# Kernel optimization log

Hardware: AMD Instinct MI355X
Metric: run time of the kernel (lower is better)

## Reference

```python
import jax, jax.numpy as jnp
import numpy as np

D_MODEL = 3072
N_HEADS = 24
HEAD_DIM = D_MODEL // N_HEADS          # 128
Q_PROJ = D_MODEL // 2                  # 1536
KV_PROJ = 2 * D_MODEL // 3             # 2048
ROPE_DIM = HEAD_DIM // 2               # 64 (qk_rope_dim == qk_no_rope_dim)
MAX_LEN = 2048
ROPE_THETA = 10000.0
EPS = 1e-6
B, S = 2, 2048


def setup_inputs() -> dict:
    key = jax.random.key(0)
    ks = jax.random.split(key, 7)
    return {
        "x": jax.random.normal(ks[0], (B, S, D_MODEL), dtype=jnp.float32),
        "scale": jnp.ones((D_MODEL,), dtype=jnp.float32),
        "w_dq": 0.01 * jax.random.normal(ks[1], (D_MODEL, Q_PROJ), dtype=jnp.float32),
        "w_uq": 0.01 * jax.random.normal(ks[2], (Q_PROJ, D_MODEL), dtype=jnp.float32),
        "w_dkv": 0.01 * jax.random.normal(ks[3], (D_MODEL, KV_PROJ + ROPE_DIM), dtype=jnp.float32),
        "w_ukv": 0.01 * jax.random.normal(ks[4], (KV_PROJ, D_MODEL + N_HEADS * ROPE_DIM), dtype=jnp.float32),
        "w_o": 0.01 * jax.random.normal(ks[5], (D_MODEL, D_MODEL), dtype=jnp.float32),
    }


def _rope_cos_sin(seq_len):
    # freqs over full head_dim, sliced to rope_dim//2 then tiled x2 (as in torch repeat)
    freqs = 1.0 / (ROPE_THETA ** (jnp.arange(0, HEAD_DIM, 2, dtype=jnp.float32) / HEAD_DIM))
    angles = jnp.arange(seq_len, dtype=jnp.float32)[:, None] * freqs[None, :]  # [S, 64]
    ang = angles[:, : ROPE_DIM // 2]                                            # [S, 32]
    cos = jnp.tile(jnp.cos(ang), (1, 2))                                        # [S, 64]
    sin = jnp.tile(jnp.sin(ang), (1, 2))
    return cos[None, None], sin[None, None]  # [1,1,S,64]


def _rotate_half(t):
    a, b = jnp.split(t, 2, axis=-1)
    return jnp.concatenate([-b, a], axis=-1)


def reference(x, scale, w_dq, w_uq, w_dkv, w_ukv, w_o):
    b, s, _ = x.shape
    # RMSNorm pre-normalization
    xn = scale * (x * jax.lax.rsqrt(jnp.mean(x * x, axis=-1, keepdims=True) + EPS))
    # two-stage query projection
    q = (xn @ w_dq) @ w_uq                                   # [B,S,D]
    q = q.reshape(b, s, N_HEADS, HEAD_DIM).transpose(0, 2, 1, 3)  # [B,H,S,hd]
    q_no_rope, q_rope = jnp.split(q, [ROPE_DIM], axis=-1)
    cos, sin = _rope_cos_sin(s)
    q_rope = q_rope * cos + _rotate_half(q_rope) * sin
    # KV down projection (this is the kv cache)
    kv_down = xn @ w_dkv                                     # [B,S,KV_PROJ+rope]
    kv_no_rope, k_rope = jnp.split(kv_down, [KV_PROJ], axis=-1)
    # KV up projection
    kv_up = kv_no_rope @ w_ukv                               # [B,S,H*(hd+rope)]
    kv_up = kv_up.reshape(b, s, N_HEADS, HEAD_DIM + ROPE_DIM).transpose(0, 2, 1, 3)
    key, value = jnp.split(kv_up, [ROPE_DIM], axis=-1)       # key [B,H,S,64], value [B,H,S,128]
    # shared rope key (one head, broadcast to all heads)
    k_rope = k_rope[:, None, :, :]                           # [B,1,S,64]
    k_rope = k_rope * cos + _rotate_half(k_rope) * sin
    k_rope = jnp.broadcast_to(k_rope, (b, N_HEADS, s, ROPE_DIM))
    final_q = jnp.concatenate([q_no_rope, q_rope], axis=-1)  # [B,H,S,128]
    final_k = jnp.concatenate([key, k_rope], axis=-1)        # [B,H,S,128]
    # masked SDPA (causal, past_length=0)
    inv_scale = 1.0 / jnp.sqrt(jnp.asarray(HEAD_DIM, dtype=x.dtype))
    scores = jnp.einsum("bhsd,bhtd->bhst", final_q, final_k) * inv_scale
    causal = jnp.tril(jnp.ones((s, s), dtype=bool))
    scores = jnp.where(causal[None, None], scores, jnp.asarray(-1e30, dtype=scores.dtype))
    attn = jax.nn.softmax(scores, axis=-1)
    attn_out = jnp.einsum("bhst,bhtd->bhsd", attn, value)    # [B,H,S,128]
    attn_out = attn_out.transpose(0, 2, 1, 3).reshape(b, s, D_MODEL)
    output = attn_out @ w_o.T
    return output, kv_down
```

## Files before the change

### kernel.cpp

```cpp
#include <hip/hip_runtime.h>
#include <hip/hip_bf16.h>
#include <stdint.h>

using bf16_t = __bf16;
using bf16x8 = __attribute__((ext_vector_type(8))) __bf16;
using bf16x4 = __attribute__((ext_vector_type(4))) __bf16;
using f32x4  = __attribute__((ext_vector_type(4))) float;

#define D_MODEL 3072
#define N_HEADS 24
#define HEAD_DIM 128
#define Q_PROJ 1536
#define KV_PROJ 2048
#define ROPE_DIM 64
#define S_LEN 2048
#define NTOK 4096
#define KVDN 2112
#define KVUN 4608

__device__ __forceinline__ void async_ld16(const void* g, void* l) {
    __builtin_amdgcn_global_load_lds(
        (__attribute__((address_space(1))) uint32_t*)(uintptr_t)g,
        (__attribute__((address_space(3))) uint32_t*)(uint32_t)(uintptr_t)l,
        16, 0, 0);
}

#define BARRIER() __builtin_amdgcn_s_barrier()
#define WAITV0() asm volatile("s_waitcnt vmcnt(0)" ::: "memory")

__global__ __launch_bounds__(256) void rmsnorm_kernel(
    const float* __restrict__ x, const float* __restrict__ sc, bf16_t* __restrict__ xn)
{
    const int tok = blockIdx.x;
    const int t = threadIdx.x;
    const float4* xr = (const float4*)(x + (size_t)tok * D_MODEL);
    float4 a = xr[t], b = xr[t + 256], c = xr[t + 512];
    float ss = a.x*a.x + a.y*a.y + a.z*a.z + a.w*a.w
             + b.x*b.x + b.y*b.y + b.z*b.z + b.w*b.w
             + c.x*c.x + c.y*c.y + c.z*c.z + c.w*c.w;
    #pragma unroll
    for (int off = 32; off >= 1; off >>= 1) ss += __shfl_xor(ss, off);
    __shared__ float red[4];
    if ((t & 63) == 0) red[t >> 6] = ss;
    __syncthreads();
    const float inv = rsqrtf((red[0] + red[1] + red[2] + red[3]) * (1.0f / D_MODEL) + 1e-6f);
    const float4* sr = (const float4*)sc;
    float4 s0 = sr[t], s1 = sr[t + 256], s2 = sr[t + 512];
    bf16x4* xo = (bf16x4*)(xn + (size_t)tok * D_MODEL);
    bf16x4 o;
    o[0]=(bf16_t)(a.x*s0.x*inv); o[1]=(bf16_t)(a.y*s0.y*inv); o[2]=(bf16_t)(a.z*s0.z*inv); o[3]=(bf16_t)(a.w*s0.w*inv);
    xo[t] = o;
    o[0]=(bf16_t)(b.x*s1.x*inv); o[1]=(bf16_t)(b.y*s1.y*inv); o[2]=(bf16_t)(b.z*s1.z*inv); o[3]=(bf16_t)(b.w*s1.w*inv);
    xo[t + 256] = o;
    o[0]=(bf16_t)(c.x*s2.x*inv); o[1]=(bf16_t)(c.y*s2.y*inv); o[2]=(bf16_t)(c.z*s2.z*inv); o[3]=(bf16_t)(c.w*s2.w*inv);
    xo[t + 512] = o;
}

__global__ void transpose_conv(const float* __restrict__ in, bf16_t* __restrict__ out, int K, int N)
{
    __shared__ float tile[32][33];
    const int n0 = blockIdx.x * 32, k0 = blockIdx.y * 32;
    const int tx = threadIdx.x, ty = threadIdx.y;
    #pragma unroll
    for (int i = 0; i < 32; i += 8)
        tile[ty + i][tx] = in[(size_t)(k0 + ty + i) * N + n0 + tx];
    __syncthreads();
    #pragma unroll
    for (int i = 0; i < 32; i += 8)
        out[(size_t)(n0 + ty + i) * K + k0 + tx] = (bf16_t)tile[tx][ty + i];
}

__global__ void conv_bf16(const float* __restrict__ in, bf16_t* __restrict__ out, int n4)
{
    const int stride = gridDim.x * 256;
    for (int i = blockIdx.x * 256 + threadIdx.x; i < n4; i += stride) {
        float4 v = ((const float4*)in)[i];
        bf16x4 o;
        o[0] = (bf16_t)v.x; o[1] = (bf16_t)v.y; o[2] = (bf16_t)v.z; o[3] = (bf16_t)v.w;
        ((bf16x4*)out)[i] = o;
    }
}

template<int RH, int BNF>
__device__ __forceinline__ void mfmaQ(f32x4 (&acc)[8][BNF], const bf16x8 (&af)[4],
                                      const bf16x8 (&bfv)[BNF]) {
    __builtin_amdgcn_s_setprio(1);
    #pragma unroll
    for (int i = 0; i < 4; ++i)
        #pragma unroll
        for (int cf = 0; cf < BNF; ++cf)
            acc[RH*4+i][cf] = __builtin_amdgcn_mfma_f32_16x16x32_bf16(af[i], bfv[cf], acc[RH*4+i][cf], 0, 0, 0);
    __builtin_amdgcn_s_setprio(0);
}

template<int BNF>
__global__ __launch_bounds__(512, 2) void gemm256(
    const bf16_t* __restrict__ A, const bf16_t* __restrict__ B, int N, int K,
    float* __restrict__ Cf, int ldf, int flo, int fhi,
    bf16_t* __restrict__ Cb1, int ldb1, int b1lo, int b1hi,
    bf16_t* __restrict__ Cb2, int ldb2, int b2lo, int b2hi,
    bf16_t* __restrict__ vt)
{
    constexpr int BN = BNF * 64;
    constexpr uint32_t BSLOT = BNF * 4096;
    __shared__ char LDS[65536 + 4 * BSLOT];
    char* Lc = LDS;
    const int tid = threadIdx.x;
    const int wv = tid >> 6, lane = tid & 63;
    const int fr = lane & 15, fg = lane >> 4;
    const int wr = wv >> 2, wc = wv & 3;

    int lin = blockIdx.y * gridDim.x + blockIdx.x;
    const int nwg = gridDim.x * gridDim.y;
    if ((nwg & 7) == 0) lin = (lin & 7) * (nwg >> 3) + (lin >> 3);
    const int bx = lin % gridDim.x, by = lin / gridDim.x;
    const int m0 = by << 8, n0 = bx * BN;

    const uint32_t slot4 = (uint32_t)((fg ^ ((fr >> 1) & 3)) << 4);

    const bf16_t* agp[2]; const bf16_t* bgp[2];
    uint32_t aoff[2], boff[2];
    #pragma unroll
    for (int j = 0; j < 2; ++j) {
        const int c = j * 512 + tid;
        const int g = c ^ ((c >> 3) & 3);
        agp[j] = A + (size_t)(m0 + (g >> 2)) * K + (g & 3) * 8;
        aoff[j] = (uint32_t)((j * 8 + wv) * 1024);
        const int cb = j * (BNF * 128) + tid;
        const int gb = cb ^ ((cb >> 3) & 3);
        int br = n0 + (gb >> 2); if (br > N - 1) br = N - 1;
        bgp[j] = B + (size_t)br * K + (gb & 3) * 8;
        boff[j] = (uint32_t)(j * (BNF * 2048) + wv * 1024);
    }

    f32x4 acc[8][BNF];
    f32x4 zero = {0.f, 0.f, 0.f, 0.f};
    #pragma unroll
    for (int i = 0; i < 8; ++i)
        #pragma unroll
        for (int j = 0; j < BNF; ++j) acc[i][j] = zero;

    bf16x8 A0[4], A1[4], B0[BNF], B1[BNF];
    const int rowA = (wr << 7) + fr;
    const int rowB = wc * (BNF * 16) + fr;

    auto stA = [&](int t, int kh) {
        const uint32_t sb = (uint32_t)(((2*t + kh) & 3) << 14);
        #pragma unroll
        for (int j = 0; j < 2; ++j)
            async_ld16(agp[j] + t * 64 + kh * 32, Lc + sb + aoff[j]);
    };
    auto stB = [&](int t, int kh) {
        const uint32_t sb = 65536u + (uint32_t)(((2*t + kh) & 3) * BSLOT);
        if (tid < BNF * 128) {
            #pragma unroll
            for (int j = 0; j < 2; ++j)
                async_ld16(bgp[j] + t * 64 + kh * 32, Lc + sb + boff[j]);
        }
    };
    auto ldA4 = [&](int t, int kh, int rh, bf16x8 (&dst)[4]) {
        const uint32_t base = (uint32_t)(((2*t + kh) & 3) << 14);
        #pragma unroll
        for (int i = 0; i < 4; ++i)
            dst[i] = *(const bf16x8*)(Lc + base + (rowA + (rh * 4 + i) * 16) * 64 + slot4);
    };
    auto ldBn = [&](int t, int kh, bf16x8 (&dst)[BNF]) {
        const uint32_t base = 65536u + (uint32_t)(((2*t + kh) & 3) * BSLOT);
        #pragma unroll
        for (int cf = 0; cf < BNF; ++cf)
            dst[cf] = *(const bf16x8*)(Lc + base + (rowB + cf * 16) * 64 + slot4);
    };

    const int NT = K >> 6;
    stA(0, 0); stB(0, 0); stA(0, 1); stB(0, 1);
    WAITV0(); BARRIER();
    ldA4(0, 0, 0, A0); ldBn(0, 0, B0);

    for (int t = 0; t < NT; ++t) {
        const bool pref = (t < NT - 1);
        ldA4(t, 0, 1, A1);
        if (pref) { stA(t + 1, 0); stB(t + 1, 0); }
        mfmaQ<0, BNF>(acc, A0, B0);
        BARRIER();
        ldA4(t, 1, 0, A0); ldBn(t, 1, B1);
        if (pref) { stA(t + 1, 1); stB(t + 1, 1); }
        mfmaQ<1, BNF>(acc, A1, B0);
        BARRIER();
        ldA4(t, 1, 1, A1);
        mfmaQ<0, BNF>(acc, A0, B1);
        if (pref) WAITV0();
        BARRIER();
        if (pref) { ldA4(t + 1, 0, 0, A0); ldBn(t + 1, 0, B0); }
        mfmaQ<1, BNF>(acc, A1, B1);
        BARRIER();
    }

    const int colb = n0 + wc * (BNF * 16) + fr;
    const int rowb = m0 + (wr << 7) + fg * 4;
    if (vt) {
        #pragma unroll
        for (int rf = 0; rf < 8; ++rf) {
            const int row0 = rowb + rf * 16;
            const int bb = row0 >> 11, s0 = row0 & 2047;
            #pragma unroll
            for (int cf = 0; cf < BNF; ++cf) {
                const int col = colb + cf * 16;
                const int h = col / 192;
                const int dm = col - h * 192;
                if (dm < 64) {
                    #pragma unroll
                    for (int r = 0; r < 4; ++r)
                        Cb1[(size_t)(row0 + r) * ldb1 + col] = (bf16_t)acc[rf][cf][r];
                } else {
                    bf16x4 o;
                    o[0] = (bf16_t)acc[rf][cf][0];
                    o[1] = (bf16_t)acc[rf][cf][1];
                    o[2] = (bf16_t)acc[rf][cf][2];
                    o[3] = (bf16_t)acc[rf][cf][3];
                    *(bf16x4*)(vt + ((size_t)((bb * 24 + h) * 128 + dm - 64)) * 2048 + s0) = o;
                }
            }
        }
    } else {
        #pragma unroll
        for (int rf = 0; rf < 8; ++rf)
            #pragma unroll
            for (int cf = 0; cf < BNF; ++cf) {
                const int col = colb + cf * 16;
                #pragma unroll
                for (int r = 0; r < 4; ++r) {
                    const int row = rowb + rf * 16 + r;
                    const float v = acc[rf][cf][r];
                    if (Cf  && col >= flo  && col < fhi)  Cf [(size_t)row * ldf  + col - flo]  = v;
                    if (Cb1 && col >= b1lo && col < b1hi) Cb1[(size_t)row * ldb1 + col - b1lo] = (bf16_t)v;
                    if (Cb2 && col >= b2lo && col < b2hi) Cb2[(size_t)row * ldb2 + col - b2lo] = (bf16_t)v;
                }
            }
    }
}

__global__ void rope_tab(float* __restrict__ ctab, float* __restrict__ stab)
{
    const int idx = blockIdx.x * 256 + threadIdx.x;
    if (idx >= S_LEN * 32) return;
    const int s = idx >> 5, i = idx & 31;
    const float freq = powf(10000.0f, -(float)(2 * i) * (1.0f / 128.0f));
    const float ang = (float)s * freq;
    ctab[idx] = cosf(ang);
    stab[idx] = sinf(ang);
}

__global__ void rope_q_kernel(bf16_t* __restrict__ q, const float* __restrict__ ctab,
                              const float* __restrict__ stab)
{
    const int idx = blockIdx.x * 256 + threadIdx.x;
    if (idx >= NTOK * N_HEADS * 32) return;
    const int i = idx & 31;
    const int rest = idx >> 5;
    const int h = rest % N_HEADS;
    const int tok = rest / N_HEADS;
    const int s = tok & (S_LEN - 1);
    bf16_t* p = q + (size_t)tok * D_MODEL + h * HEAD_DIM + 64;
    const float a = (float)p[i], b = (float)p[i + 32];
    const float c = ctab[s * 32 + i], sn = stab[s * 32 + i];
    p[i]      = (bf16_t)(a * c - b * sn);
    p[i + 32] = (bf16_t)(b * c + a * sn);
}

__global__ void rope_k_kernel(const float* __restrict__ kvd, bf16_t* __restrict__ kr,
                              const float* __restrict__ ctab, const float* __restrict__ stab)
{
    const int idx = blockIdx.x * 256 + threadIdx.x;
    if (idx >= NTOK * 32) return;
    const int i = idx & 31;
    const int tok = idx >> 5;
    const int s = tok & (S_LEN - 1);
    const float* p = kvd + (size_t)tok * KVDN + KV_PROJ;
    const float a = p[i], b = p[i + 32];
    const float c = ctab[s * 32 + i], sn = stab[s * 32 + i];
    kr[(size_t)tok * 64 + i]      = (bf16_t)(a * c - b * sn);
    kr[(size_t)tok * 64 + i + 32] = (bf16_t)(b * c + a * sn);
}

__global__ __launch_bounds__(256, 2) void attn_fwd(
    const bf16_t* __restrict__ Q, const bf16_t* __restrict__ KVUP,
    const bf16_t* __restrict__ KR, const bf16_t* __restrict__ VT,
    bf16_t* __restrict__ AO)
{
    __shared__ bf16_t Knr[2][64 * 64];
    __shared__ bf16_t Krp[2][64 * 64];
    __shared__ bf16_t Vls[2][128 * 64];

    const int bh = blockIdx.y;
    const int b = bh / N_HEADS, h = bh % N_HEADS;
    const int wave = threadIdx.x >> 6, lane = threadIdx.x & 63;
    const int fr = lane & 15, fg = lane >> 4;
    const int rx = fr & 7;
    const int hi = fg >> 1;
    const int s0l = fr + 32 * (fg & 1);
    const int s1l = s0l + 16;

    const bf16_t* Kb  = KVUP + (size_t)b * S_LEN * KVUN + (size_t)h * 192;
    const bf16_t* KRb = KR + (size_t)b * S_LEN * 64;
    const bf16_t* Vb  = VT + (size_t)bh * HEAD_DIM * S_LEN;

    const int srow   = lane >> 3;
    const int schunk = (lane & 7) ^ srow;
    const float l2e_isc = 0.127500625f;

    f32x4 zero = {0.f, 0.f, 0.f, 0.f};

    #pragma unroll 1
    for (int tp = 0; tp < 2; ++tp) {
        const int qt = (tp == 0) ? blockIdx.x : (15 - blockIdx.x);
        const int qb = qt * 128;
        const int wrow0 = qb + wave * 32;

        bf16x8 qf[2][4];
        #pragma unroll
        for (int rf = 0; rf < 2; ++rf)
            #pragma unroll
            for (int kc = 0; kc < 4; ++kc)
                qf[rf][kc] = *(const bf16x8*)(Q + (size_t)(b * S_LEN + wrow0 + rf * 16 + fr) * D_MODEL
                                              + h * HEAD_DIM + kc * 32 + fg * 8);
        f32x4 oacc[2][8];
        float m_i[2], l_i[2];
        #pragma unroll
        for (int rf = 0; rf < 2; ++rf) {
            #pragma unroll
            for (int nf = 0; nf < 8; ++nf) oacc[rf][nf] = zero;
            m_i[rf] = -1e30f; l_i[rf] = 0.f;
        }

        auto stage = [&](int kvb, int bf) {
            #pragma unroll
            for (int c = 0; c < 2; ++c) {
                const int r0 = wave * 16 + c * 8;
                async_ld16(Kb  + (size_t)(kvb + r0 + srow) * KVUN + schunk * 8, &Knr[bf][r0 * 64]);
                async_ld16(KRb + (size_t)(kvb + r0 + srow) * 64   + schunk * 8, &Krp[bf][r0 * 64]);
            }
            #pragma unroll
            for (int c = 0; c < 4; ++c) {
                const int r0 = wave * 32 + c * 8;
                async_ld16(Vb + (size_t)(r0 + srow) * S_LEN + kvb + schunk * 8, &Vls[bf][r0 * 64]);
            }
        };

        const int kvend = qb + 128;
        int cur = 0;
        stage(0, 0);
        __syncthreads();

        #pragma unroll 1
        for (int kvb = 0; kvb < kvend; kvb += 64) {
            if (kvb + 64 < kvend) stage(kvb + 64, cur ^ 1);

            if (kvb <= wrow0 + 31) {
                const bf16_t* Kc = Knr[cur];
                const bf16_t* Rc = Krp[cur];
                const bf16_t* Vc = Vls[cur];

                f32x4 sacc[2][4];
                #pragma unroll
                for (int rf = 0; rf < 2; ++rf)
                    #pragma unroll
                    for (int jn = 0; jn < 4; ++jn) sacc[rf][jn] = zero;
                __builtin_amdgcn_s_setprio(1);
                #pragma unroll
                for (int jn = 0; jn < 4; ++jn) {
                    const int krow = jn * 16 + fr;
                    bf16x8 kA = *(const bf16x8*)(Kc + krow * 64 + (((0 + fg) ^ rx) << 3));
                    bf16x8 kB = *(const bf16x8*)(Kc + krow * 64 + (((4 + fg) ^ rx) << 3));
                    bf16x8 kC = *(const bf16x8*)(Rc + krow * 64 + (((0 + fg) ^ rx) << 3));
                    bf16x8 kD = *(const bf16x8*)(Rc + krow * 64 + (((4 + fg) ^ rx) << 3));
                    #pragma unroll
                    for (int rf = 0; rf < 2; ++rf) {
                        sacc[rf][jn] = __builtin_amdgcn_mfma_f32_16x16x32_bf16(kA, qf[rf][0], sacc[rf][jn], 0, 0, 0);
                        sacc[rf][jn] = __builtin_amdgcn_mfma_f32_16x16x32_bf16(kB, qf[rf][1], sacc[rf][jn], 0, 0, 0);
                        sacc[rf][jn] = __builtin_amdgcn_mfma_f32_16x16x32_bf16(kC, qf[rf][2], sacc[rf][jn], 0, 0, 0);
                        sacc[rf][jn] = __builtin_amdgcn_mfma_f32_16x16x32_bf16(kD, qf[rf][3], sacc[rf][jn], 0, 0, 0);
                    }
                }
                __builtin_amdgcn_s_setprio(0);

                const bool needMask = (kvb + 63 > wrow0);
                uint32_t pk[2][4][2];
                float scf[2];
                #pragma unroll
                for (int rf = 0; rf < 2; ++rf) {
                    const int qrow = wrow0 + rf * 16 + fr;
                    float mx = -1e30f;
                    #pragma unroll
                    for (int jn = 0; jn < 4; ++jn)
                        #pragma unroll
                        for (int r = 0; r < 4; ++r) {
                            float v = sacc[rf][jn][r] * l2e_isc;
                            if (needMask && (kvb + jn * 16 + fg * 4 + r > qrow)) v = -1e30f;
                            sacc[rf][jn][r] = v;
                            mx = fmaxf(mx, v);
                        }
                    mx = fmaxf(mx, __shfl_xor(mx, 16));
                    mx = fmaxf(mx, __shfl_xor(mx, 32));
                    const float mn = fmaxf(m_i[rf], mx);
                    scf[rf] = __builtin_amdgcn_exp2f(m_i[rf] - mn);
                    m_i[rf] = mn;
                    float ls = 0.f;
                    #pragma unroll
                    for (int jn = 0; jn < 4; ++jn) {
                        float p0 = __builtin_amdgcn_exp2f(sacc[rf][jn][0] - mn);
                        float p1 = __builtin_amdgcn_exp2f(sacc[rf][jn][1] - mn);
                        float p2 = __builtin_amdgcn_exp2f(sacc[rf][jn][2] - mn);
                        float p3 = __builtin_amdgcn_exp2f(sacc[rf][jn][3] - mn);
                        ls += (p0 + p1) + (p2 + p3);
                        union { bf16x4 h; uint32_t w[2]; } cv;
                        cv.h[0] = (bf16_t)p0; cv.h[1] = (bf16_t)p1;
                        cv.h[2] = (bf16_t)p2; cv.h[3] = (bf16_t)p3;
                        pk[rf][jn][0] = cv.w[0]; pk[rf][jn][1] = cv.w[1];
                    }
                    ls += __shfl_xor(ls, 16);
                    ls += __shfl_xor(ls, 32);
                    l_i[rf] = l_i[rf] * scf[rf] + ls;
                    #pragma unroll
                    for (int nf = 0; nf < 8; ++nf)
                        #pragma unroll
                        for (int r = 0; r < 4; ++r) oacc[rf][nf][r] *= scf[rf];
                }

                bf16x8 bfr[2][2];
                #pragma unroll
                for (int rf = 0; rf < 2; ++rf)
                    #pragma unroll
                    for (int ks = 0; ks < 2; ++ks) {
                        const uint32_t t00 = __shfl(pk[rf][2*ks][0],   s0l);
                        const uint32_t t01 = __shfl(pk[rf][2*ks][1],   s0l);
                        const uint32_t t10 = __shfl(pk[rf][2*ks+1][0], s0l);
                        const uint32_t t11 = __shfl(pk[rf][2*ks+1][1], s0l);
                        const uint32_t u00 = __shfl(pk[rf][2*ks][0],   s1l);
                        const uint32_t u01 = __shfl(pk[rf][2*ks][1],   s1l);
                        const uint32_t u10 = __shfl(pk[rf][2*ks+1][0], s1l);
                        const uint32_t u11 = __shfl(pk[rf][2*ks+1][1], s1l);
                        union { bf16x8 h; uint32_t w[4]; } bb;
                        bb.w[0] = hi ? t10 : t00;
                        bb.w[1] = hi ? t11 : t01;
                        bb.w[2] = hi ? u10 : u00;
                        bb.w[3] = hi ? u11 : u01;
                        bfr[rf][ks] = bb.h;
                    }

                __builtin_amdgcn_s_setprio(1);
                #pragma unroll
                for (int nf = 0; nf < 8; ++nf) {
                    const int vrow = nf * 16 + fr;
                    bf16x8 v0 = *(const bf16x8*)(Vc + vrow * 64 + (((0 + fg) ^ rx) << 3));
                    bf16x8 v1 = *(const bf16x8*)(Vc + vrow * 64 + (((4 + fg) ^ rx) << 3));
                    #pragma unroll
                    for (int rf = 0; rf < 2; ++rf) {
                        oacc[rf][nf] = __builtin_amdgcn_mfma_f32_16x16x32_bf16(v0, bfr[rf][0], oacc[rf][nf], 0, 0, 0);
                        oacc[rf][nf] = __builtin_amdgcn_mfma_f32_16x16x32_bf16(v1, bfr[rf][1], oacc[rf][nf], 0, 0, 0);
                    }
                }
                __builtin_amdgcn_s_setprio(0);
            }
            __syncthreads();
            cur ^= 1;
        }

        #pragma unroll
        for (int rf = 0; rf < 2; ++rf) {
            const float rl = __builtin_amdgcn_rcpf(l_i[rf]);
            const int qrow = wrow0 + rf * 16 + fr;
            bf16_t* aob = AO + (size_t)(b * S_LEN + qrow) * D_MODEL + h * HEAD_DIM + fg * 4;
            #pragma unroll
            for (int nf = 0; nf < 8; ++nf) {
                bf16x4 o;
                o[0] = (bf16_t)(oacc[rf][nf][0] * rl);
                o[1] = (bf16_t)(oacc[rf][nf][1] * rl);
                o[2] = (bf16_t)(oacc[rf][nf][2] * rl);
                o[3] = (bf16_t)(oacc[rf][nf][3] * rl);
                *(bf16x4*)(aob + nf * 16) = o;
            }
        }
    }
}

extern "C" void kernel_launch(void* const* d_in, const int* in_sizes, int n_in,
                              void* d_out, int out_size, void* d_ws, size_t ws_size,
                              hipStream_t stream)
{
    const float* x     = (const float*)d_in[0];
    const float* scale = (const float*)d_in[1];
    const float* w_dq  = (const float*)d_in[2];
    const float* w_uq  = (const float*)d_in[3];
    const float* w_dkv = (const float*)d_in[4];
    const float* w_ukv = (const float*)d_in[5];
    const float* w_o   = (const float*)d_in[6];
    float* out0 = (float*)d_out;
    float* out1 = out0 + (size_t)NTOK * D_MODEL;

    if (ws_size < 187039744ull) return;
    char* ws = (char*)d_ws;
    bf16_t* XN    = (bf16_t*)(ws + 0);
    bf16_t* WCAT  = (bf16_t*)(ws + 25165824ull);
    bf16_t* WUQT  = (bf16_t*)(ws + 47579136ull);
    bf16_t* WUKVT = (bf16_t*)(ws + 57016320ull);
    bf16_t* WOB   = (bf16_t*)(ws + 75890688ull);
    bf16_t* QD    = (bf16_t*)(ws + 94765056ull);
    bf16_t* Qb    = (bf16_t*)(ws + 107347968ull);
    bf16_t* KVNR  = (bf16_t*)(ws + 132513792ull);
    bf16_t* KVUP  = (bf16_t*)(ws + 149291008ull);
    bf16_t* KRB   = (bf16_t*)(ws + 94765056ull);
    float*  CTAB  = (float*) (ws + 95289344ull);
    float*  STAB  = (float*) (ws + 95551488ull);
    bf16_t* VTb   = WCAT;
    bf16_t* AO    = XN;

    rmsnorm_kernel<<<NTOK, 256, 0, stream>>>(x, scale, XN);
    transpose_conv<<<dim3(1536/32, 3072/32), dim3(32,8), 0, stream>>>(w_dq,  WCAT, 3072, 1536);
    transpose_conv<<<dim3(2112/32, 3072/32), dim3(32,8), 0, stream>>>(w_dkv, WCAT + (size_t)1536*3072, 3072, 2112);
    transpose_conv<<<dim3(3072/32, 1536/32), dim3(32,8), 0, stream>>>(w_uq,  WUQT, 1536, 3072);
    transpose_conv<<<dim3(4608/32, 2048/32), dim3(32,8), 0, stream>>>(w_ukv, WUKVT, 2048, 4608);
    conv_bf16<<<2048, 256, 0, stream>>>(w_o, WOB, (D_MODEL * D_MODEL) / 4);

    gemm256<4><<<dim3(15, 16), 512, 0, stream>>>(XN, WCAT, 3648, 3072,
        out1, KVDN, 1536, 3648,
        QD,   Q_PROJ, 0, 1536,
        KVNR, KV_PROJ, 1536, 3584, nullptr);
    gemm256<3><<<dim3(16, 16), 512, 0, stream>>>(QD, WUQT, 3072, 1536,
        nullptr, 0, 0, 0, Qb, D_MODEL, 0, 3072, nullptr, 0, 0, 0, nullptr);
    rope_tab<<<(S_LEN * 32 + 255) / 256, 256, 0, stream>>>(CTAB, STAB);
    rope_q_kernel<<<(NTOK * N_HEADS * 32 + 255) / 256, 256, 0, stream>>>(Qb, CTAB, STAB);
    rope_k_kernel<<<(NTOK * 32 + 255) / 256, 256, 0, stream>>>(out1, KRB, CTAB, STAB);
    gemm256<3><<<dim3(24, 16), 512, 0, stream>>>(KVNR, WUKVT, 4608, 2048,
        nullptr, 0, 0, 0, KVUP, KVUN, 0, 0, nullptr, 0, 0, 0, VTb);
    attn_fwd<<<dim3(8, 48), 256, 0, stream>>>(Qb, KVUP, KRB, VTb, AO);
    gemm256<3><<<dim3(16, 16), 512, 0, stream>>>(AO, WOB, 3072, 3072,
        out0, D_MODEL, 0, 3072, nullptr, 0, 0, 0, nullptr, 0, 0, 0, nullptr);
}
```

Baseline: 537.6 us.

## Deepen GEMM prefetch to two tiles, fold softmax scale into Q, lazy rescale

The GEMM now issues global-to-LDS loads two K-tiles ahead and waits with partial vmcnt counts (different per wave role), replacing the full drain each iteration so memory latency overlaps more compute. The log2e/sqrt(d) softmax scale is folded into the Q up-projection epilogue, which removes a per-score multiply in attention. Attention also skips the online-softmax rescale of the output accumulator unless the row max grows by more than a threshold, trading rare extra work for fewer multiplies. Risks include subtle vmcnt miscounting, since the counts depend on how many loads each wave issues, and reduced bf16 precision from scaling Q before rounding.

```diff
diff --git a/kernel.cpp b/kernel.cpp
--- a/kernel.cpp
+++ b/kernel.cpp
@@ -26,7 +26,7 @@
 }
 
 #define BARRIER() __builtin_amdgcn_s_barrier()
-#define WAITV0() asm volatile("s_waitcnt vmcnt(0)" ::: "memory")
+#define WAITVN(n) asm volatile("s_waitcnt vmcnt(" #n ")" ::: "memory")
 
 __global__ __launch_bounds__(256) void rmsnorm_kernel(
     const float* __restrict__ x, const float* __restrict__ sc, bf16_t* __restrict__ xn)
@@ -99,7 +99,7 @@
     float* __restrict__ Cf, int ldf, int flo, int fhi,
     bf16_t* __restrict__ Cb1, int ldb1, int b1lo, int b1hi,
     bf16_t* __restrict__ Cb2, int ldb2, int b2lo, int b2hi,
-    bf16_t* __restrict__ vt)
+    bf16_t* __restrict__ vt, float cbscale)
 {
     constexpr int BN = BNF * 64;
     constexpr uint32_t BSLOT = BNF * 4096;
@@ -109,6 +109,7 @@
     const int wv = tid >> 6, lane = tid & 63;
     const int fr = lane & 15, fg = lane >> 4;
     const int wr = wv >> 2, wc = wv & 3;
+    const bool bwave = (wv < 2 * BNF);
 
     int lin = blockIdx.y * gridDim.x + blockIdx.x;
     const int nwg = gridDim.x * gridDim.y;
@@ -173,24 +174,27 @@
 
     const int NT = K >> 6;
     stA(0, 0); stB(0, 0); stA(0, 1); stB(0, 1);
-    WAITV0(); BARRIER();
+    stA(1, 0); stB(1, 0); stA(1, 1); stB(1, 1);
+    if (bwave) { WAITVN(8); } else { WAITVN(4); }
+    BARRIER();
     ldA4(0, 0, 0, A0); ldBn(0, 0, B0);
 
     for (int t = 0; t < NT; ++t) {
-        const bool pref = (t < NT - 1);
+        const bool pref = (t + 2 < NT);
         ldA4(t, 0, 1, A1);
-        if (pref) { stA(t + 1, 0); stB(t + 1, 0); }
         mfmaQ<0, BNF>(acc, A0, B0);
+        if (pref) { if (bwave) { WAITVN(4); } else { WAITVN(2); } }
+        else      { WAITVN(0); }
         BARRIER();
         ldA4(t, 1, 0, A0); ldBn(t, 1, B1);
-        if (pref) { stA(t + 1, 1); stB(t + 1, 1); }
+        if (pref) { stA(t + 2, 0); stB(t + 2, 0); }
         mfmaQ<1, BNF>(acc, A1, B0);
         BARRIER();
         ldA4(t, 1, 1, A1);
         mfmaQ<0, BNF>(acc, A0, B1);
-        if (pref) WAITV0();
         BARRIER();
-        if (pref) { ldA4(t + 1, 0, 0, A0); ldBn(t + 1, 0, B0); }
+        if (t + 1 < NT) { ldA4(t + 1, 0, 0, A0); ldBn(t + 1, 0, B0); }
+        if (pref) { stA(t + 2, 1); stB(t + 2, 1); }
         mfmaQ<1, BNF>(acc, A1, B1);
         BARRIER();
     }
@@ -232,7 +236,7 @@
                     const int row = rowb + rf * 16 + r;
                     const float v = acc[rf][cf][r];
                     if (Cf  && col >= flo  && col < fhi)  Cf [(size_t)row * ldf  + col - flo]  = v;
-                    if (Cb1 && col >= b1lo && col < b1hi) Cb1[(size_t)row * ldb1 + col - b1lo] = (bf16_t)v;
+                    if (Cb1 && col >= b1lo && col < b1hi) Cb1[(size_t)row * ldb1 + col - b1lo] = (bf16_t)(v * cbscale);
                     if (Cb2 && col >= b2lo && col < b2hi) Cb2[(size_t)row * ldb2 + col - b2lo] = (bf16_t)v;
                 }
             }
@@ -306,7 +310,6 @@
 
     const int srow   = lane >> 3;
     const int schunk = (lane & 7) ^ srow;
-    const float l2e_isc = 0.127500625f;
 
     f32x4 zero = {0.f, 0.f, 0.f, 0.f};
 
@@ -385,7 +388,6 @@
 
                 const bool needMask = (kvb + 63 > wrow0);
                 uint32_t pk[2][4][2];
-                float scf[2];
                 #pragma unroll
                 for (int rf = 0; rf < 2; ++rf) {
                     const int qrow = wrow0 + rf * 16 + fr;
@@ -394,16 +396,24 @@
                     for (int jn = 0; jn < 4; ++jn)
                         #pragma unroll
                         for (int r = 0; r < 4; ++r) {
-                            float v = sacc[rf][jn][r] * l2e_isc;
+                            float v = sacc[rf][jn][r];
                             if (needMask && (kvb + jn * 16 + fg * 4 + r > qrow)) v = -1e30f;
                             sacc[rf][jn][r] = v;
                             mx = fmaxf(mx, v);
                         }
                     mx = fmaxf(mx, __shfl_xor(mx, 16));
                     mx = fmaxf(mx, __shfl_xor(mx, 32));
-                    const float mn = fmaxf(m_i[rf], mx);
-                    scf[rf] = __builtin_amdgcn_exp2f(m_i[rf] - mn);
-                    m_i[rf] = mn;
+                    if (!__all(mx <= m_i[rf] + 8.f)) {
+                        const float mn = fmaxf(m_i[rf], mx);
+                        const float sc = __builtin_amdgcn_exp2f(m_i[rf] - mn);
+                        m_i[rf] = mn;
+                        l_i[rf] *= sc;
+                        #pragma unroll
+                        for (int nf = 0; nf < 8; ++nf)
+                            #pragma unroll
+                            for (int r = 0; r < 4; ++r) oacc[rf][nf][r] *= sc;
+                    }
+                    const float mn = m_i[rf];
                     float ls = 0.f;
                     #pragma unroll
                     for (int jn = 0; jn < 4; ++jn) {
@@ -419,11 +429,7 @@
                     }
                     ls += __shfl_xor(ls, 16);
                     ls += __shfl_xor(ls, 32);
-                    l_i[rf] = l_i[rf] * scf[rf] + ls;
-                    #pragma unroll
-                    for (int nf = 0; nf < 8; ++nf)
-                        #pragma unroll
-                        for (int r = 0; r < 4; ++r) oacc[rf][nf][r] *= scf[rf];
+                    l_i[rf] += ls;
                 }
 
                 bf16x8 bfr[2][2];
@@ -514,6 +520,8 @@
     bf16_t* VTb   = WCAT;
     bf16_t* AO    = XN;
 
+    const float l2e_isc = 0.127500625f;
+
     rmsnorm_kernel<<<NTOK, 256, 0, stream>>>(x, scale, XN);
     transpose_conv<<<dim3(1536/32, 3072/32), dim3(32,8), 0, stream>>>(w_dq,  WCAT, 3072, 1536);
     transpose_conv<<<dim3(2112/32, 3072/32), dim3(32,8), 0, stream>>>(w_dkv, WCAT + (size_t)1536*3072, 3072, 2112);
@@ -524,15 +532,15 @@
     gemm256<4><<<dim3(15, 16), 512, 0, stream>>>(XN, WCAT, 3648, 3072,
         out1, KVDN, 1536, 3648,
         QD,   Q_PROJ, 0, 1536,
-        KVNR, KV_PROJ, 1536, 3584, nullptr);
+        KVNR, KV_PROJ, 1536, 3584, nullptr, 1.0f);
     gemm256<3><<<dim3(16, 16), 512, 0, stream>>>(QD, WUQT, 3072, 1536,
-        nullptr, 0, 0, 0, Qb, D_MODEL, 0, 3072, nullptr, 0, 0, 0, nullptr);
+        nullptr, 0, 0, 0, Qb, D_MODEL, 0, 3072, nullptr, 0, 0, 0, nullptr, l2e_isc);
     rope_tab<<<(S_LEN * 32 + 255) / 256, 256, 0, stream>>>(CTAB, STAB);
     rope_q_kernel<<<(NTOK * N_HEADS * 32 + 255) / 256, 256, 0, stream>>>(Qb, CTAB, STAB);
     rope_k_kernel<<<(NTOK * 32 + 255) / 256, 256, 0, stream>>>(out1, KRB, CTAB, STAB);
     gemm256<3><<<dim3(24, 16), 512, 0, stream>>>(KVNR, WUKVT, 4608, 2048,
-        nullptr, 0, 0, 0, KVUP, KVUN, 0, 0, nullptr, 0, 0, 0, VTb);
+        nullptr, 0, 0, 0, KVUP, KVUN, 0, 0, nullptr, 0, 0, 0, VTb, 1.0f);
     attn_fwd<<<dim3(8, 48), 256, 0, stream>>>(Qb, KVUP, KRB, VTb, AO);
     gemm256<3><<<dim3(16, 16), 512, 0, stream>>>(AO, WOB, 3072, 3072,
-        out0, D_MODEL, 0, 3072, nullptr, 0, 0, 0, nullptr, 0, 0, 0, nullptr);
-}
+        out0, D_MODEL, 0, 3072, nullptr, 0, 0, 0, nullptr, 0, 0, 0, nullptr, 1.0f);
+}
```

Result: faster. 521.7 us (-3.0%).
